# Kernel optimization log

Hardware: AMD Instinct MI355X
Metric: run time of the kernel (lower is better)

The kernel has to match this reference:

```python
import jax, jax.numpy as jnp
import numpy as np

N = 100000   # nodes
E = 1250000  # directed edges
F = 32       # node_features
H = 64       # hidden_channels
C = 10       # num_classes
NEG_SLOPE = 0.2  # GATConv default LeakyReLU slope


def _glorot(key, shape):
    fan_in = shape[0]
    return jax.random.normal(key, shape, jnp.float32) / np.sqrt(fan_in)


def setup_inputs() -> dict:
    k = jax.random.split(jax.random.key(0), 16)
    x = jax.random.normal(k[0], (N, F), jnp.float32)
    edge_index = jax.random.randint(k[1], (2, E), 0, N, dtype=jnp.int32)
    return {
        "x": x,
        "edge_index": edge_index,
        # GCNConv 1
        "W1": _glorot(k[2], (F, H)), "b1": jnp.zeros((H,), jnp.float32),
        # GATConv (heads=1)
        "W2": _glorot(k[3], (H, H)),
        "a_src": _glorot(k[4], (H,)), "a_dst": _glorot(k[5], (H,)),
        "b2": jnp.zeros((H,), jnp.float32),
        # GCNConv 3
        "W3": _glorot(k[6], (H, H)), "b3": jnp.zeros((H,), jnp.float32),
        # optimization head
        "Wopt": _glorot(k[7], (H, C)), "bopt": jnp.zeros((C,), jnp.float32),
        # bottleneck detector MLP
        "Wb1": _glorot(k[8], (H, 32)), "bb1": jnp.zeros((32,), jnp.float32),
        "Wb2": _glorot(k[9], (32, 1)), "bb2": jnp.zeros((1,), jnp.float32),
    }


def _gcn_conv(x, W, b, src, dst, n):
    # PyG GCNConv: self-loops already appended to src/dst by caller.
    h = x @ W  # [n, out]
    deg = jnp.zeros((n,), x.dtype).at[dst].add(1.0)
    dinv = jax.lax.rsqrt(jnp.maximum(deg, 1e-12))
    norm = dinv[src] * dinv[dst]  # [e]
    msg = h[src] * norm[:, None]  # gather + scale
    out = jnp.zeros_like(h).at[dst].add(msg)  # scatter-add
    return out + b


def _gat_conv(x, W, a_src, a_dst, b, src, dst, n):
    # PyG GATConv, heads=1: self-loops already appended.
    h = x @ W  # [n, out]
    alpha_s = h @ a_src  # [n]
    alpha_d = h @ a_dst  # [n]
    e = jax.nn.leaky_relu(alpha_s[src] + alpha_d[dst], NEG_SLOPE)  # [e]
    # softmax over incoming edges of each dst node
    emax = jax.ops.segment_max(e, dst, num_segments=n)
    p = jnp.exp(e - emax[dst])
    denom = jax.ops.segment_sum(p, dst, num_segments=n)
    alpha = p / denom[dst]
    out = jnp.zeros_like(h).at[dst].add(h[src] * alpha[:, None])
    return out + b


def reference(x, edge_index, W1, b1, W2, a_src, a_dst, b2, W3, b3,
              Wopt, bopt, Wb1, bb1, Wb2, bb2):
    n = x.shape[0]
    loops = jnp.arange(n, dtype=edge_index.dtype)
    src = jnp.concatenate([edge_index[0], loops])
    dst = jnp.concatenate([edge_index[1], loops])

    h = jax.nn.relu(_gcn_conv(x, W1, b1, src, dst, n))
    h = jax.nn.relu(_gat_conv(h, W2, a_src, a_dst, b2, src, dst, n))
    h = jax.nn.relu(_gcn_conv(h, W3, b3, src, dst, n))

    optimizations = h @ Wopt + bopt                     # [n, C]
    bottlenecks = jax.nn.sigmoid(jax.nn.relu(h @ Wb1 + bb1) @ Wb2 + bb2)  # [n, 1]
    graph_embedding = h.mean(axis=0)                    # [H]
    return optimizations, bottlenecks, graph_embedding
```

## Files before the change

kernel.cpp:

```cpp
#include <hip/hip_runtime.h>
#include <hip/hip_bf16.h>


#define CAP 64
#define NBUK 8

typedef unsigned uvec4 __attribute__((ext_vector_type(4)));

__device__ __forceinline__ int uwave(){
  return __builtin_amdgcn_readfirstlane(threadIdx.x >> 6);
}
__device__ __forceinline__ unsigned short f2bf(float f){
  unsigned u = __float_as_uint(f);
  return (unsigned short)((u + 0x7fffu + ((u >> 16) & 1u)) >> 16);
}
__device__ __forceinline__ float bfl(unsigned u){ return __uint_as_float(u << 16); }
__device__ __forceinline__ float bfh(unsigned u){ return __uint_as_float(u & 0xffff0000u); }

__global__ void k_setup(const float* __restrict__ Wopt, const float* __restrict__ bopt,
                        const float* __restrict__ Wb1, const float* __restrict__ bb1,
                        float* __restrict__ Wcat, float* __restrict__ bcat,
                        int* __restrict__ cnt, int* __restrict__ bcnt,
                        unsigned short* __restrict__ tb,
                        unsigned short* __restrict__ xh, float* __restrict__ emb_acc,
                        int n){
  int i = blockIdx.x*blockDim.x + threadIdx.x;
  if (i < n) cnt[i] = 0;
  if (blockIdx.x == 0){
    int tid = threadIdx.x;
    for (int j = tid; j < 4096; j += 256){
      int f = j >> 6, c = j & 63;
      float w = 0.f;
      if (c < 10)       w = Wopt[f*10 + c];
      else if (c >= 32) w = Wb1[f*32 + (c-32)];
      Wcat[j] = w;
    }
    if (tid < 64){
      float b = 0.f;
      if (tid < 10)       b = bopt[tid];
      else if (tid >= 32) b = bb1[tid-32];
      bcat[tid] = b;
      tb[(size_t)n*64 + tid] = 0;
      emb_acc[tid] = 0.f;
    }
    if (tid >= 64 && tid < 96) xh[(size_t)n*32 + (tid-64)] = 0;
    if (tid >= 96 && tid < 96 + NBUK) bcnt[tid-96] = 0;
  }
}

__global__ __launch_bounds__(256) void k_part(const int* __restrict__ src,
                        const int* __restrict__ dst,
                        uint2* __restrict__ pairs, int* __restrict__ bcnt,
                        int e, int pbcap, float binv){
  __shared__ int lcnt[NBUK];
  __shared__ int lbase[NBUK];
  int tid = threadIdx.x;
  if (tid < NBUK) lcnt[tid] = 0;
  __syncthreads();
  int i0 = blockIdx.x*1024 + tid*4;
  int d[4], s[4], bk[4], lp[4];
  int nv = e - i0;
  if (nv > 4) nv = 4;
  if (nv == 4){
    int4 dd = *(const int4*)(dst + i0);
    int4 ss = *(const int4*)(src + i0);
    d[0]=dd.x; d[1]=dd.y; d[2]=dd.z; d[3]=dd.w;
    s[0]=ss.x; s[1]=ss.y; s[2]=ss.z; s[3]=ss.w;
  } else {
    #pragma unroll
    for (int j = 0; j < 4; j++){ d[j] = 0; s[j] = 0; }
    for (int j = 0; j < nv; j++){ d[j] = dst[i0+j]; s[j] = src[i0+j]; }
  }
  #pragma unroll
  for (int j = 0; j < 4; j++){
    if (j < nv){
      bk[j] = min(NBUK-1, (int)((float)d[j] * binv));
      lp[j] = atomicAdd(&lcnt[bk[j]], 1);
    }
  }
  __syncthreads();
  if (tid < NBUK) lbase[tid] = atomicAdd(&bcnt[tid], lcnt[tid]);
  __syncthreads();
  #pragma unroll
  for (int j = 0; j < 4; j++){
    if (j < nv){
      int p = lbase[bk[j]] + lp[j];
      if (p < pbcap)
        pairs[(size_t)bk[j]*pbcap + p] = make_uint2((unsigned)d[j], (unsigned)s[j]);
    }
  }
}

__global__ __launch_bounds__(256) void k_fill(const uint2* __restrict__ pairs,
                        const int* __restrict__ bcnt, int* __restrict__ cnt,
                        int* __restrict__ adj, int pbcap){
  int b = blockIdx.x & (NBUK-1);
  int m = bcnt[b];
  if (m > pbcap) m = pbcap;
  const uvec4* pb = (const uvec4*)(pairs + (size_t)b*pbcap);
  int half = (m + 1) >> 1;
  int tpb = (gridDim.x >> 3) * 256;
  for (int j = (blockIdx.x >> 3)*256 + threadIdx.x; j < half; j += tpb){
    uvec4 p = __builtin_nontemporal_load(pb + j);
    int pos0 = atomicAdd(&cnt[p.x], 1);
    bool ok1 = (2*j + 1) < m;
    int pos1 = ok1 ? atomicAdd(&cnt[p.z], 1) : 0;
    if (pos0 < CAP) adj[(size_t)p.x*CAP + pos0] = (int)p.y;
    if (ok1 && pos1 < CAP) adj[(size_t)p.z*CAP + pos1] = (int)p.w;
  }
}

__global__ void k_castscale(const float* __restrict__ x, const int* __restrict__ cnt,
                            unsigned short* __restrict__ xh, int total4){
  int i = blockIdx.x*blockDim.x + threadIdx.x;
  if (i >= total4) return;
  int row = i >> 3;
  float dv = rsqrtf((float)(cnt[row] + 1));
  float4 v = ((const float4*)x)[i];
  uint2 o;
  o.x = (unsigned)f2bf(v.x*dv) | ((unsigned)f2bf(v.y*dv) << 16);
  o.y = (unsigned)f2bf(v.z*dv) | ((unsigned)f2bf(v.w*dv) << 16);
  ((uint2*)xh)[i] = o;
}

__global__ __launch_bounds__(256) void k_agg32g(const unsigned short* __restrict__ xh,
                          const int* __restrict__ adj, const int* __restrict__ cnt,
                          const float* __restrict__ W1, const float* __restrict__ b1,
                          unsigned short* __restrict__ h, int n){
  int lane = threadIdx.x & 63;
  float wreg[32];
  #pragma unroll
  for (int k = 0; k < 32; k++) wreg[k] = W1[k*64 + lane];
  float br = b1[lane];
  int v0 = blockIdx.x*8 + uwave()*2;
  if (v0 >= n) return;
  int v1 = v0 + 1;
  bool has1 = v1 < n;
  if (!has1) v1 = v0;
  int cn0 = cnt[v0], cn1 = cnt[v1];
  int c0 = min(cn0, CAP), c1 = min(cn1, CAP);
  int ureg0 = n, ureg1 = n;
  if (lane < c0) ureg0 = (adj + (size_t)v0*CAP)[lane];
  if (lane < c1) ureg1 = (adj + (size_t)v1*CAP)[lane];
  int g = lane >> 3, q = lane & 7;
  float4 a0 = {0.f,0.f,0.f,0.f}, a1 = {0.f,0.f,0.f,0.f};
  int itm = (max(c0, c1) + 7) >> 3;
  #pragma unroll 2
  for (int jj = 0; jj < itm; jj++){
    int u0 = __shfl(ureg0, jj*8 + g);
    int u1 = __shfl(ureg1, jj*8 + g);
    uint2 r0 = ((const uint2*)(xh + (size_t)u0*32))[q];
    uint2 r1 = ((const uint2*)(xh + (size_t)u1*32))[q];
    a0.x += bfl(r0.x); a0.y += bfh(r0.x); a0.z += bfl(r0.y); a0.w += bfh(r0.y);
    a1.x += bfl(r1.x); a1.y += bfh(r1.x); a1.z += bfl(r1.y); a1.w += bfh(r1.y);
  }
  #pragma unroll
  for (int off = 8; off <= 32; off <<= 1){
    a0.x += __shfl_xor(a0.x, off); a0.y += __shfl_xor(a0.y, off);
    a0.z += __shfl_xor(a0.z, off); a0.w += __shfl_xor(a0.w, off);
    a1.x += __shfl_xor(a1.x, off); a1.y += __shfl_xor(a1.y, off);
    a1.z += __shfl_xor(a1.z, off); a1.w += __shfl_xor(a1.w, off);
  }
  uint2 s0 = ((const uint2*)(xh + (size_t)v0*32))[q];
  uint2 s1 = ((const uint2*)(xh + (size_t)v1*32))[q];
  a0.x += bfl(s0.x); a0.y += bfh(s0.x); a0.z += bfl(s0.y); a0.w += bfh(s0.y);
  a1.x += bfl(s1.x); a1.y += bfh(s1.x); a1.z += bfl(s1.y); a1.w += bfh(s1.y);
  float dv0 = rsqrtf((float)(cn0 + 1)), dv1 = rsqrtf((float)(cn1 + 1));
  a0.x *= dv0; a0.y *= dv0; a0.z *= dv0; a0.w *= dv0;
  a1.x *= dv1; a1.y *= dv1; a1.z *= dv1; a1.w *= dv1;
  float h0 = br, h1v = br;
  #pragma unroll
  for (int q2 = 0; q2 < 8; q2++){
    float4 w0, w1;
    w0.x = __shfl(a0.x, q2); w0.y = __shfl(a0.y, q2);
    w0.z = __shfl(a0.z, q2); w0.w = __shfl(a0.w, q2);
    w1.x = __shfl(a1.x, q2); w1.y = __shfl(a1.y, q2);
    w1.z = __shfl(a1.z, q2); w1.w = __shfl(a1.w, q2);
    h0 = fmaf(w0.x, wreg[q2*4+0], h0); h1v = fmaf(w1.x, wreg[q2*4+0], h1v);
    h0 = fmaf(w0.y, wreg[q2*4+1], h0); h1v = fmaf(w1.y, wreg[q2*4+1], h1v);
    h0 = fmaf(w0.z, wreg[q2*4+2], h0); h1v = fmaf(w1.z, wreg[q2*4+2], h1v);
    h0 = fmaf(w0.w, wreg[q2*4+3], h0); h1v = fmaf(w1.w, wreg[q2*4+3], h1v);
  }
  h[(size_t)v0*64 + lane] = f2bf(fmaxf(h0, 0.f));
  if (has1) h[(size_t)v1*64 + lane] = f2bf(fmaxf(h1v, 0.f));
}

template<bool SCALE>
__global__ __launch_bounds__(256, 4) void k_gemm_b(const unsigned short* __restrict__ x,
                       const float* __restrict__ W, const int* __restrict__ cnt,
                       unsigned short* __restrict__ t, int n){
  int lane = threadIdx.x & 63;
  int gw = blockIdx.x*4 + uwave();
  int nw = gridDim.x*4;
  float wreg[64];
  #pragma unroll
  for (int k = 0; k < 64; k++) wreg[k] = W[k*64 + lane];
  for (int v = gw; v < n; v += nw){
    const uint4* xr = (const uint4*)(x + (size_t)v*64);
    float acc = 0.f;
    #pragma unroll
    for (int k8 = 0; k8 < 8; k8++){
      uint4 c = xr[k8];
      acc = fmaf(bfl(c.x), wreg[k8*8+0], acc);
      acc = fmaf(bfh(c.x), wreg[k8*8+1], acc);
      acc = fmaf(bfl(c.y), wreg[k8*8+2], acc);
      acc = fmaf(bfh(c.y), wreg[k8*8+3], acc);
      acc = fmaf(bfl(c.z), wreg[k8*8+4], acc);
      acc = fmaf(bfh(c.z), wreg[k8*8+5], acc);
      acc = fmaf(bfl(c.w), wreg[k8*8+6], acc);
      acc = fmaf(bfh(c.w), wreg[k8*8+7], acc);
    }
    if (SCALE) acc *= rsqrtf((float)(cnt[v] + 1));
    t[(size_t)v*64 + lane] = f2bf(acc);
  }
}

__global__ __launch_bounds__(256, 4) void k_gemm_alpha(const unsigned short* __restrict__ x,
                       const float* __restrict__ W,
                       const float* __restrict__ asrc, const float* __restrict__ adst,
                       unsigned short* __restrict__ t, float* __restrict__ als,
                       float* __restrict__ ald, int n){
  int lane = threadIdx.x & 63;
  int gw = blockIdx.x*4 + uwave();
  int nw = gridDim.x*4;
  float wreg[64];
  #pragma unroll
  for (int k = 0; k < 64; k++) wreg[k] = W[k*64 + lane];
  float asr = asrc[lane], adr = adst[lane];
  for (int v = gw; v < n; v += nw){
    const uint4* xr = (const uint4*)(x + (size_t)v*64);
    float acc = 0.f;
    #pragma unroll
    for (int k8 = 0; k8 < 8; k8++){
      uint4 c = xr[k8];
      acc = fmaf(bfl(c.x), wreg[k8*8+0], acc);
      acc = fmaf(bfh(c.x), wreg[k8*8+1], acc);
      acc = fmaf(bfl(c.y), wreg[k8*8+2], acc);
      acc = fmaf(bfh(c.y), wreg[k8*8+3], acc);
      acc = fmaf(bfl(c.z), wreg[k8*8+4], acc);
      acc = fmaf(bfh(c.z), wreg[k8*8+5], acc);
      acc = fmaf(bfl(c.w), wreg[k8*8+6], acc);
      acc = fmaf(bfh(c.w), wreg[k8*8+7], acc);
    }
    t[(size_t)v*64 + lane] = f2bf(acc);
    float s1 = acc * asr, s2 = acc * adr;
    #pragma unroll
    for (int off = 32; off; off >>= 1){
      s1 += __shfl_xor(s1, off);
      s2 += __shfl_xor(s2, off);
    }
    if (lane == 0){ als[v] = s1; ald[v] = s2; }
  }
}

__global__ __launch_bounds__(256) void k_gcn_agg(const unsigned short* __restrict__ t,
                          const int* __restrict__ adj, const int* __restrict__ cnt,
                          const float* __restrict__ b, unsigned short* __restrict__ h, int n){
  int lane = threadIdx.x & 63;
  int v0 = blockIdx.x*8 + uwave()*2;
  if (v0 >= n) return;
  int v1 = v0 + 1;
  bool has1 = v1 < n;
  if (!has1) v1 = v0;
  int cn0 = cnt[v0], cn1 = cnt[v1];
  int c0 = min(cn0, CAP), c1 = min(cn1, CAP);
  int ureg0 = n, ureg1 = n;
  if (lane < c0) ureg0 = (adj + (size_t)v0*CAP)[lane];
  if (lane < c1) ureg1 = (adj + (size_t)v1*CAP)[lane];
  int g = lane >> 3, q = lane & 7;
  float a0[8] = {0,0,0,0,0,0,0,0}, a1[8] = {0,0,0,0,0,0,0,0};
  int itm = (max(c0, c1) + 7) >> 3;
  #pragma unroll 2
  for (int jj = 0; jj < itm; jj++){
    int u0 = __shfl(ureg0, jj*8 + g);
    int u1 = __shfl(ureg1, jj*8 + g);
    uint4 r0 = ((const uint4*)(t + (size_t)u0*64))[q];
    uint4 r1 = ((const uint4*)(t + (size_t)u1*64))[q];
    a0[0] += bfl(r0.x); a0[1] += bfh(r0.x); a0[2] += bfl(r0.y); a0[3] += bfh(r0.y);
    a0[4] += bfl(r0.z); a0[5] += bfh(r0.z); a0[6] += bfl(r0.w); a0[7] += bfh(r0.w);
    a1[0] += bfl(r1.x); a1[1] += bfh(r1.x); a1[2] += bfl(r1.y); a1[3] += bfh(r1.y);
    a1[4] += bfl(r1.z); a1[5] += bfh(r1.z); a1[6] += bfl(r1.w); a1[7] += bfh(r1.w);
  }
  #pragma unroll
  for (int off = 8; off <= 32; off <<= 1){
    #pragma unroll
    for (int k = 0; k < 8; k++){
      a0[k] += __shfl_xor(a0[k], off);
      a1[k] += __shfl_xor(a1[k], off);
    }
  }
  uint4 s0 = ((const uint4*)(t + (size_t)v0*64))[q];
  uint4 s1 = ((const uint4*)(t + (size_t)v1*64))[q];
  a0[0] += bfl(s0.x); a0[1] += bfh(s0.x); a0[2] += bfl(s0.y); a0[3] += bfh(s0.y);
  a0[4] += bfl(s0.z); a0[5] += bfh(s0.z); a0[6] += bfl(s0.w); a0[7] += bfh(s0.w);
  a1[0] += bfl(s1.x); a1[1] += bfh(s1.x); a1[2] += bfl(s1.y); a1[3] += bfh(s1.y);
  a1[4] += bfl(s1.z); a1[5] += bfh(s1.z); a1[6] += bfl(s1.w); a1[7] += bfh(s1.w);
  float dv0 = rsqrtf((float)(cn0 + 1)), dv1 = rsqrtf((float)(cn1 + 1));
  float4 b0 = ((const float4*)b)[2*q], b1v = ((const float4*)b)[2*q+1];
  if (g == 0){
    float r0 = fmaxf(fmaf(a0[0], dv0, b0.x), 0.f),  r1 = fmaxf(fmaf(a0[1], dv0, b0.y), 0.f);
    float r2 = fmaxf(fmaf(a0[2], dv0, b0.z), 0.f),  r3 = fmaxf(fmaf(a0[3], dv0, b0.w), 0.f);
    float r4 = fmaxf(fmaf(a0[4], dv0, b1v.x), 0.f), r5 = fmaxf(fmaf(a0[5], dv0, b1v.y), 0.f);
    float r6 = fmaxf(fmaf(a0[6], dv0, b1v.z), 0.f), r7 = fmaxf(fmaf(a0[7], dv0, b1v.w), 0.f);
    uint4 o;
    o.x = (unsigned)f2bf(r0) | ((unsigned)f2bf(r1) << 16);
    o.y = (unsigned)f2bf(r2) | ((unsigned)f2bf(r3) << 16);
    o.z = (unsigned)f2bf(r4) | ((unsigned)f2bf(r5) << 16);
    o.w = (unsigned)f2bf(r6) | ((unsigned)f2bf(r7) << 16);
    ((uint4*)(h + (size_t)v0*64))[q] = o;
  } else if (g == 1 && has1){
    float r0 = fmaxf(fmaf(a1[0], dv1, b0.x), 0.f),  r1 = fmaxf(fmaf(a1[1], dv1, b0.y), 0.f);
    float r2 = fmaxf(fmaf(a1[2], dv1, b0.z), 0.f),  r3 = fmaxf(fmaf(a1[3], dv1, b0.w), 0.f);
    float r4 = fmaxf(fmaf(a1[4], dv1, b1v.x), 0.f), r5 = fmaxf(fmaf(a1[5], dv1, b1v.y), 0.f);
    float r6 = fmaxf(fmaf(a1[6], dv1, b1v.z), 0.f), r7 = fmaxf(fmaf(a1[7], dv1, b1v.w), 0.f);
    uint4 o;
    o.x = (unsigned)f2bf(r0) | ((unsigned)f2bf(r1) << 16);
    o.y = (unsigned)f2bf(r2) | ((unsigned)f2bf(r3) << 16);
    o.z = (unsigned)f2bf(r4) | ((unsigned)f2bf(r5) << 16);
    o.w = (unsigned)f2bf(r6) | ((unsigned)f2bf(r7) << 16);
    ((uint4*)(h + (size_t)v1*64))[q] = o;
  }
}

__global__ __launch_bounds__(256) void k_gat_agg(const unsigned short* __restrict__ t,
                          const int* __restrict__ adj, const int* __restrict__ cnt,
                          const float* __restrict__ als, const float* __restrict__ ald,
                          const float* __restrict__ b, unsigned short* __restrict__ h, int n){
  int lane = threadIdx.x & 63;
  int v0 = blockIdx.x*8 + uwave()*2;
  if (v0 >= n) return;
  int v1 = v0 + 1;
  bool has1 = v1 < n;
  if (!has1) v1 = v0;
  int c0 = min(cnt[v0], CAP), c1 = min(cnt[v1], CAP);
  int ureg0 = n, ureg1 = n;
  if (lane < c0) ureg0 = (adj + (size_t)v0*CAP)[lane];
  if (lane < c1) ureg1 = (adj + (size_t)v1*CAP)[lane];
  int us0 = (lane < c0) ? ureg0 : v0;
  int us1 = (lane < c1) ? ureg1 : v1;
  float adv0 = ald[v0], adv1 = ald[v1];
  float e0 = als[us0] + adv0;
  float e1 = als[us1] + adv1;
  e0 = e0 > 0.f ? e0 : 0.2f*e0;
  e1 = e1 > 0.f ? e1 : 0.2f*e1;
  float es0 = als[v0] + adv0; es0 = es0 > 0.f ? es0 : 0.2f*es0;
  float es1 = als[v1] + adv1; es1 = es1 > 0.f ? es1 : 0.2f*es1;
  float em0 = (lane < c0) ? e0 : -1e30f;
  float em1 = (lane < c1) ? e1 : -1e30f;
  #pragma unroll
  for (int off = 32; off; off >>= 1){
    em0 = fmaxf(em0, __shfl_xor(em0, off));
    em1 = fmaxf(em1, __shfl_xor(em1, off));
  }
  em0 = fmaxf(em0, es0); em1 = fmaxf(em1, es1);
  float p0 = (lane < c0) ? __expf(e0 - em0) : 0.f;
  float p1 = (lane < c1) ? __expf(e1 - em1) : 0.f;
  float sm0 = p0, sm1 = p1;
  #pragma unroll
  for (int off = 32; off; off >>= 1){
    sm0 += __shfl_xor(sm0, off);
    sm1 += __shfl_xor(sm1, off);
  }
  float ps0 = __expf(es0 - em0), ps1 = __expf(es1 - em1);
  float inv0 = 1.f / (sm0 + ps0), inv1 = 1.f / (sm1 + ps1);
  int g = lane >> 3, q = lane & 7;
  float a0[8] = {0,0,0,0,0,0,0,0}, a1[8] = {0,0,0,0,0,0,0,0};
  int itm = (max(c0, c1) + 7) >> 3;
  #pragma unroll 2
  for (int jj = 0; jj < itm; jj++){
    int   u0 = __shfl(ureg0, jj*8 + g);
    int   u1 = __shfl(ureg1, jj*8 + g);
    float w0 = __shfl(p0,    jj*8 + g);
    float w1 = __shfl(p1,    jj*8 + g);
    uint4 r0 = ((const uint4*)(t + (size_t)u0*64))[q];
    uint4 r1 = ((const uint4*)(t + (size_t)u1*64))[q];
    a0[0] = fmaf(w0, bfl(r0.x), a0[0]); a0[1] = fmaf(w0, bfh(r0.x), a0[1]);
    a0[2] = fmaf(w0, bfl(r0.y), a0[2]); a0[3] = fmaf(w0, bfh(r0.y), a0[3]);
    a0[4] = fmaf(w0, bfl(r0.z), a0[4]); a0[5] = fmaf(w0, bfh(r0.z), a0[5]);
    a0[6] = fmaf(w0, bfl(r0.w), a0[6]); a0[7] = fmaf(w0, bfh(r0.w), a0[7]);
    a1[0] = fmaf(w1, bfl(r1.x), a1[0]); a1[1] = fmaf(w1, bfh(r1.x), a1[1]);
    a1[2] = fmaf(w1, bfl(r1.y), a1[2]); a1[3] = fmaf(w1, bfh(r1.y), a1[3]);
    a1[4] = fmaf(w1, bfl(r1.z), a1[4]); a1[5] = fmaf(w1, bfh(r1.z), a1[5]);
    a1[6] = fmaf(w1, bfl(r1.w), a1[6]); a1[7] = fmaf(w1, bfh(r1.w), a1[7]);
  }
  #pragma unroll
  for (int off = 8; off <= 32; off <<= 1){
    #pragma unroll
    for (int k = 0; k < 8; k++){
      a0[k] += __shfl_xor(a0[k], off);
      a1[k] += __shfl_xor(a1[k], off);
    }
  }
  uint4 s0 = ((const uint4*)(t + (size_t)v0*64))[q];
  uint4 s1 = ((const uint4*)(t + (size_t)v1*64))[q];
  a0[0] = fmaf(ps0, bfl(s0.x), a0[0]); a0[1] = fmaf(ps0, bfh(s0.x), a0[1]);
  a0[2] = fmaf(ps0, bfl(s0.y), a0[2]); a0[3] = fmaf(ps0, bfh(s0.y), a0[3]);
  a0[4] = fmaf(ps0, bfl(s0.z), a0[4]); a0[5] = fmaf(ps0, bfh(s0.z), a0[5]);
  a0[6] = fmaf(ps0, bfl(s0.w), a0[6]); a0[7] = fmaf(ps0, bfh(s0.w), a0[7]);
  a1[0] = fmaf(ps1, bfl(s1.x), a1[0]); a1[1] = fmaf(ps1, bfh(s1.x), a1[1]);
  a1[2] = fmaf(ps1, bfl(s1.y), a1[2]); a1[3] = fmaf(ps1, bfh(s1.y), a1[3]);
  a1[4] = fmaf(ps1, bfl(s1.z), a1[4]); a1[5] = fmaf(ps1, bfh(s1.z), a1[5]);
  a1[6] = fmaf(ps1, bfl(s1.w), a1[6]); a1[7] = fmaf(ps1, bfh(s1.w), a1[7]);
  float4 b0 = ((const float4*)b)[2*q], b1v = ((const float4*)b)[2*q+1];
  if (g == 0){
    float r0 = fmaxf(fmaf(a0[0], inv0, b0.x), 0.f),  r1 = fmaxf(fmaf(a0[1], inv0, b0.y), 0.f);
    float r2 = fmaxf(fmaf(a0[2], inv0, b0.z), 0.f),  r3 = fmaxf(fmaf(a0[3], inv0, b0.w), 0.f);
    float r4 = fmaxf(fmaf(a0[4], inv0, b1v.x), 0.f), r5 = fmaxf(fmaf(a0[5], inv0, b1v.y), 0.f);
    float r6 = fmaxf(fmaf(a0[6], inv0, b1v.z), 0.f), r7 = fmaxf(fmaf(a0[7], inv0, b1v.w), 0.f);
    uint4 o;
    o.x = (unsigned)f2bf(r0) | ((unsigned)f2bf(r1) << 16);
    o.y = (unsigned)f2bf(r2) | ((unsigned)f2bf(r3) << 16);
    o.z = (unsigned)f2bf(r4) | ((unsigned)f2bf(r5) << 16);
    o.w = (unsigned)f2bf(r6) | ((unsigned)f2bf(r7) << 16);
    ((uint4*)(h + (size_t)v0*64))[q] = o;
  } else if (g == 1 && has1){
    float r0 = fmaxf(fmaf(a1[0], inv1, b0.x), 0.f),  r1 = fmaxf(fmaf(a1[1], inv1, b0.y), 0.f);
    float r2 = fmaxf(fmaf(a1[2], inv1, b0.z), 0.f),  r3 = fmaxf(fmaf(a1[3], inv1, b0.w), 0.f);
    float r4 = fmaxf(fmaf(a1[4], inv1, b1v.x), 0.f), r5 = fmaxf(fmaf(a1[5], inv1, b1v.y), 0.f);
    float r6 = fmaxf(fmaf(a1[6], inv1, b1v.z), 0.f), r7 = fmaxf(fmaf(a1[7], inv1, b1v.w), 0.f);
    uint4 o;
    o.x = (unsigned)f2bf(r0) | ((unsigned)f2bf(r1) << 16);
    o.y = (unsigned)f2bf(r2) | ((unsigned)f2bf(r3) << 16);
    o.z = (unsigned)f2bf(r4) | ((unsigned)f2bf(r5) << 16);
    o.w = (unsigned)f2bf(r6) | ((unsigned)f2bf(r7) << 16);
    ((uint4*)(h + (size_t)v1*64))[q] = o;
  }
}

__global__ __launch_bounds__(256, 4) void k_heads(const unsigned short* __restrict__ h,
                        const float* __restrict__ Wcat, const float* __restrict__ bcat,
                        const float* __restrict__ Wb2, const float* __restrict__ bb2,
                        float* __restrict__ out_opt, float* __restrict__ out_bot, int n){
  int lane = threadIdx.x & 63;
  int gw = blockIdx.x*4 + uwave();
  int nw = gridDim.x*4;
  float wreg[64];
  #pragma unroll
  for (int k = 0; k < 64; k++) wreg[k] = Wcat[k*64 + lane];
  float bcr  = bcat[lane];
  float wb2r = (lane >= 32) ? Wb2[lane-32] : 0.f;
  float bb2r = bb2[0];
  for (int v = gw; v < n; v += nw){
    const uint4* xr = (const uint4*)(h + (size_t)v*64);
    float acc = bcr;
    #pragma unroll
    for (int k8 = 0; k8 < 8; k8++){
      uint4 c = xr[k8];
      acc = fmaf(bfl(c.x), wreg[k8*8+0], acc);
      acc = fmaf(bfh(c.x), wreg[k8*8+1], acc);
      acc = fmaf(bfl(c.y), wreg[k8*8+2], acc);
      acc = fmaf(bfh(c.y), wreg[k8*8+3], acc);
      acc = fmaf(bfl(c.z), wreg[k8*8+4], acc);
      acc = fmaf(bfh(c.z), wreg[k8*8+5], acc);
      acc = fmaf(bfl(c.w), wreg[k8*8+6], acc);
      acc = fmaf(bfh(c.w), wreg[k8*8+7], acc);
    }
    if (lane < 10) out_opt[(size_t)v*10 + lane] = acc;
    float contrib = fmaxf(acc, 0.f) * wb2r;
    #pragma unroll
    for (int off = 32; off; off >>= 1) contrib += __shfl_xor(contrib, off);
    if (lane == 0) out_bot[v] = 1.f / (1.f + __expf(-(contrib + bb2r)));
  }
}

__global__ __launch_bounds__(256) void k_mean(const unsigned short* __restrict__ h,
                       float* __restrict__ emb_acc, int n){
  __shared__ float red[256];
  int tid = threadIdx.x;
  int w = tid >> 6, lane = tid & 63;
  float s = 0.f;
  for (int r = blockIdx.x*4 + w; r < n; r += 1024)
    s += __uint_as_float(((unsigned)h[(size_t)r*64 + lane]) << 16);
  red[tid] = s;
  __syncthreads();
  if (tid < 64)
    atomicAdd(&emb_acc[tid], red[tid] + red[64+tid] + red[128+tid] + red[192+tid]);
}

__global__ void k_embed(const float* __restrict__ emb_acc, float* __restrict__ out_emb,
                        float invn){
  if (threadIdx.x < 64) out_emb[threadIdx.x] = emb_acc[threadIdx.x] * invn;
}

extern "C" void kernel_launch(void* const* d_in, const int* in_sizes, int n_in,
                              void* d_out, int out_size, void* d_ws, size_t ws_size,
                              hipStream_t stream) {
  const float* x    = (const float*)d_in[0];
  const int*   ei   = (const int*)d_in[1];
  const float* W1   = (const float*)d_in[2];
  const float* b1   = (const float*)d_in[3];
  const float* W2   = (const float*)d_in[4];
  const float* a_s  = (const float*)d_in[5];
  const float* a_d  = (const float*)d_in[6];
  const float* b2   = (const float*)d_in[7];
  const float* W3   = (const float*)d_in[8];
  const float* b3   = (const float*)d_in[9];
  const float* Wopt = (const float*)d_in[10];
  const float* bopt = (const float*)d_in[11];
  const float* Wb1  = (const float*)d_in[12];
  const float* bb1  = (const float*)d_in[13];
  const float* Wb2  = (const float*)d_in[14];
  const float* bb2  = (const float*)d_in[15];

  int n = in_sizes[0] / 32;
  int e = in_sizes[1] / 2;
  const int* src = ei;
  const int* dst = ei + e;

  char* ws = (char*)d_ws;
  size_t off = 0;
  auto alloc = [&](size_t bytes) -> void* {
    void* p = ws + off;
    off += (bytes + 255) & ~(size_t)255;
    return p;
  };
  int*            cnt     = (int*)           alloc((size_t)n * 4);
  int*            adj     = (int*)           alloc((size_t)n * CAP * 4);
  float*          als     = (float*)         alloc((size_t)n * 4);
  float*          ald     = (float*)         alloc((size_t)n * 4);
  unsigned short* xh      = (unsigned short*)alloc((size_t)(n+1) * 32 * 2);
  unsigned short* tb      = (unsigned short*)alloc((size_t)(n+1) * 64 * 2);
  unsigned short* hbuf    = (unsigned short*)alloc((size_t)n * 64 * 2);
  float*          emb_acc = (float*)         alloc((size_t)64 * 4);
  float*          Wcat    = (float*)         alloc((size_t)4096 * 4);
  float*          bcat    = (float*)         alloc((size_t)64 * 4);
  int*            bcnt    = (int*)           alloc((size_t)NBUK * 4);

  int pbcap = e / NBUK + 8192;
  uint2* pairs = (uint2*)hbuf;

  float* out_opt = (float*)d_out;
  float* out_bot = out_opt + (size_t)n * 10;
  float* out_emb = out_bot + n;

  int nb8    = (n + 7) / 8;
  int nbN    = (n + 255) / 256;
  int nbP    = (e + 1023) / 1024;
  int total4 = n*32/4;
  int nbC    = (total4 + 255) / 256;

  k_setup<<<nbN, 256, 0, stream>>>(Wopt, bopt, Wb1, bb1, Wcat, bcat,
                                   cnt, bcnt, tb, xh, emb_acc, n);
  k_part<<<nbP, 256, 0, stream>>>(src, dst, pairs, bcnt, e, pbcap, 8.0f/(float)n);
  k_fill<<<2048, 256, 0, stream>>>(pairs, bcnt, cnt, adj, pbcap);
  k_castscale<<<nbC, 256, 0, stream>>>(x, cnt, xh, total4);

  k_agg32g<<<nb8, 256, 0, stream>>>(xh, adj, cnt, W1, b1, hbuf, n);

  k_gemm_alpha<<<1024, 256, 0, stream>>>(hbuf, W2, a_s, a_d, tb, als, ald, n);
  k_gat_agg<<<nb8, 256, 0, stream>>>(tb, adj, cnt, als, ald, b2, hbuf, n);

  k_gemm_b<true><<<1024, 256, 0, stream>>>(hbuf, W3, cnt, tb, n);
  k_gcn_agg<<<nb8, 256, 0, stream>>>(tb, adj, cnt, b3, hbuf, n);

  k_heads<<<1024, 256, 0, stream>>>(hbuf, Wcat, bcat, Wb2, bb2,
                                    out_opt, out_bot, n);
  k_mean<<<256, 256, 0, stream>>>(hbuf, emb_acc, n);
  k_embed<<<1, 64, 0, stream>>>(emb_acc, out_emb, 1.0f / (float)n);
}
```

Measured before the change: 413.2 us.

## Partition edges into 128-node buckets and build adjacency in shared memory

The edge partition step now buckets edges by dst>>7 into about 782 fine buckets instead of 8 coarse ones. Each fill block then builds its 128 nodes' counts and adjacency lists with LDS atomics and writes them to global memory with coalesced vector stores. This replaces global atomics on cnt and scattered adjacency writes, and removes the separate cnt zeroing. The costs are 32KB of LDS per fill block (lower occupancy), more global bucket-counter atomics in the partition step, and a tighter per-bucket pair capacity that could overflow on skewed graphs.

```diff
diff --git a/kernel.cpp b/kernel.cpp
--- a/kernel.cpp
+++ b/kernel.cpp
@@ -3,9 +3,8 @@
 
 
 #define CAP 64
-#define NBUK 8
-
-typedef unsigned uvec4 __attribute__((ext_vector_type(4)));
+#define NP2 128
+#define NB2MAX 800
 
 __device__ __forceinline__ int uwave(){
   return __builtin_amdgcn_readfirstlane(threadIdx.x >> 6);
@@ -20,12 +19,11 @@
 __global__ void k_setup(const float* __restrict__ Wopt, const float* __restrict__ bopt,
                         const float* __restrict__ Wb1, const float* __restrict__ bb1,
                         float* __restrict__ Wcat, float* __restrict__ bcat,
-                        int* __restrict__ cnt, int* __restrict__ bcnt,
-                        unsigned short* __restrict__ tb,
+                        int* __restrict__ bcnt, unsigned short* __restrict__ tb,
                         unsigned short* __restrict__ xh, float* __restrict__ emb_acc,
-                        int n){
+                        int n, int nb2){
   int i = blockIdx.x*blockDim.x + threadIdx.x;
-  if (i < n) cnt[i] = 0;
+  if (i < nb2) bcnt[i] = 0;
   if (blockIdx.x == 0){
     int tid = threadIdx.x;
     for (int j = tid; j < 4096; j += 256){
@@ -44,45 +42,50 @@
       emb_acc[tid] = 0.f;
     }
     if (tid >= 64 && tid < 96) xh[(size_t)n*32 + (tid-64)] = 0;
-    if (tid >= 96 && tid < 96 + NBUK) bcnt[tid-96] = 0;
   }
 }
 
 __global__ __launch_bounds__(256) void k_part(const int* __restrict__ src,
                         const int* __restrict__ dst,
                         uint2* __restrict__ pairs, int* __restrict__ bcnt,
-                        int e, int pbcap, float binv){
-  __shared__ int lcnt[NBUK];
-  __shared__ int lbase[NBUK];
+                        int e, int nb2, int pbcap){
+  __shared__ int lcnt[NB2MAX];
+  __shared__ int lbase[NB2MAX];
   int tid = threadIdx.x;
-  if (tid < NBUK) lcnt[tid] = 0;
+  for (int j = tid; j < nb2; j += 256) lcnt[j] = 0;
   __syncthreads();
-  int i0 = blockIdx.x*1024 + tid*4;
-  int d[4], s[4], bk[4], lp[4];
+  int i0 = blockIdx.x*2048 + tid*8;
+  int d[8], s[8], bk[8], lp[8];
   int nv = e - i0;
-  if (nv > 4) nv = 4;
-  if (nv == 4){
-    int4 dd = *(const int4*)(dst + i0);
-    int4 ss = *(const int4*)(src + i0);
-    d[0]=dd.x; d[1]=dd.y; d[2]=dd.z; d[3]=dd.w;
-    s[0]=ss.x; s[1]=ss.y; s[2]=ss.z; s[3]=ss.w;
+  if (nv > 8) nv = 8;
+  if (nv < 0) nv = 0;
+  if (nv == 8){
+    int4 d0 = *(const int4*)(dst + i0), d1 = *(const int4*)(dst + i0 + 4);
+    int4 s0 = *(const int4*)(src + i0), s1 = *(const int4*)(src + i0 + 4);
+    d[0]=d0.x; d[1]=d0.y; d[2]=d0.z; d[3]=d0.w;
+    d[4]=d1.x; d[5]=d1.y; d[6]=d1.z; d[7]=d1.w;
+    s[0]=s0.x; s[1]=s0.y; s[2]=s0.z; s[3]=s0.w;
+    s[4]=s1.x; s[5]=s1.y; s[6]=s1.z; s[7]=s1.w;
   } else {
     #pragma unroll
-    for (int j = 0; j < 4; j++){ d[j] = 0; s[j] = 0; }
+    for (int j = 0; j < 8; j++){ d[j] = 0; s[j] = 0; }
     for (int j = 0; j < nv; j++){ d[j] = dst[i0+j]; s[j] = src[i0+j]; }
   }
   #pragma unroll
-  for (int j = 0; j < 4; j++){
+  for (int j = 0; j < 8; j++){
     if (j < nv){
-      bk[j] = min(NBUK-1, (int)((float)d[j] * binv));
+      bk[j] = d[j] >> 7;
       lp[j] = atomicAdd(&lcnt[bk[j]], 1);
     }
   }
   __syncthreads();
-  if (tid < NBUK) lbase[tid] = atomicAdd(&bcnt[tid], lcnt[tid]);
+  for (int j = tid; j < nb2; j += 256){
+    int c = lcnt[j];
+    if (c) lbase[j] = atomicAdd(&bcnt[j], c);
+  }
   __syncthreads();
   #pragma unroll
-  for (int j = 0; j < 4; j++){
+  for (int j = 0; j < 8; j++){
     if (j < nv){
       int p = lbase[bk[j]] + lp[j];
       if (p < pbcap)
@@ -93,21 +96,30 @@
 
 __global__ __launch_bounds__(256) void k_fill(const uint2* __restrict__ pairs,
                         const int* __restrict__ bcnt, int* __restrict__ cnt,
-                        int* __restrict__ adj, int pbcap){
-  int b = blockIdx.x & (NBUK-1);
+                        int* __restrict__ adj, int pbcap, int n){
+  __shared__ int lc[NP2];
+  __shared__ int ladj[NP2*CAP];
+  int b = blockIdx.x;
+  int lo = b << 7;
+  int nn = min(NP2, n - lo);
+  int tid = threadIdx.x;
+  for (int j = tid; j < NP2; j += 256) lc[j] = 0;
+  __syncthreads();
   int m = bcnt[b];
   if (m > pbcap) m = pbcap;
-  const uvec4* pb = (const uvec4*)(pairs + (size_t)b*pbcap);
-  int half = (m + 1) >> 1;
-  int tpb = (gridDim.x >> 3) * 256;
-  for (int j = (blockIdx.x >> 3)*256 + threadIdx.x; j < half; j += tpb){
-    uvec4 p = __builtin_nontemporal_load(pb + j);
-    int pos0 = atomicAdd(&cnt[p.x], 1);
-    bool ok1 = (2*j + 1) < m;
-    int pos1 = ok1 ? atomicAdd(&cnt[p.z], 1) : 0;
-    if (pos0 < CAP) adj[(size_t)p.x*CAP + pos0] = (int)p.y;
-    if (ok1 && pos1 < CAP) adj[(size_t)p.z*CAP + pos1] = (int)p.w;
-  }
+  const uint2* pb = pairs + (size_t)b*pbcap;
+  for (int j = tid; j < m; j += 256){
+    uint2 p = pb[j];
+    int r = (int)p.x - lo;
+    int pos = atomicAdd(&lc[r], 1);
+    if (pos < CAP) ladj[(r << 6) + pos] = (int)p.y;
+  }
+  __syncthreads();
+  if (tid < nn) cnt[lo + tid] = lc[tid];
+  int tot = nn << 4;
+  uint4* ga = (uint4*)(adj + (size_t)lo*CAP);
+  const uint4* la = (const uint4*)ladj;
+  for (int j = tid; j < tot; j += 256) ga[j] = la[j];
 }
 
 __global__ void k_castscale(const float* __restrict__ x, const int* __restrict__ cnt,
@@ -514,6 +526,7 @@
     off += (bytes + 255) & ~(size_t)255;
     return p;
   };
+  int nb2 = (n + NP2 - 1) >> 7;
   int*            cnt     = (int*)           alloc((size_t)n * 4);
   int*            adj     = (int*)           alloc((size_t)n * CAP * 4);
   float*          als     = (float*)         alloc((size_t)n * 4);
@@ -524,9 +537,11 @@
   float*          emb_acc = (float*)         alloc((size_t)64 * 4);
   float*          Wcat    = (float*)         alloc((size_t)4096 * 4);
   float*          bcat    = (float*)         alloc((size_t)64 * 4);
-  int*            bcnt    = (int*)           alloc((size_t)NBUK * 4);
-
-  int pbcap = e / NBUK + 8192;
+  int*            bcnt    = (int*)           alloc((size_t)nb2 * 4);
+
+  int pbcap = e / nb2 + 384;
+  long pcap_max = ((long)n * 128) / ((long)nb2 * 8);
+  if (pbcap > (int)pcap_max) pbcap = (int)pcap_max;
   uint2* pairs = (uint2*)hbuf;
 
   float* out_opt = (float*)d_out;
@@ -535,14 +550,14 @@
 
   int nb8    = (n + 7) / 8;
   int nbN    = (n + 255) / 256;
-  int nbP    = (e + 1023) / 1024;
+  int nbP    = (e + 2047) / 2048;
   int total4 = n*32/4;
   int nbC    = (total4 + 255) / 256;
 
   k_setup<<<nbN, 256, 0, stream>>>(Wopt, bopt, Wb1, bb1, Wcat, bcat,
-                                   cnt, bcnt, tb, xh, emb_acc, n);
-  k_part<<<nbP, 256, 0, stream>>>(src, dst, pairs, bcnt, e, pbcap, 8.0f/(float)n);
-  k_fill<<<2048, 256, 0, stream>>>(pairs, bcnt, cnt, adj, pbcap);
+                                   bcnt, tb, xh, emb_acc, n, nb2);
+  k_part<<<nbP, 256, 0, stream>>>(src, dst, pairs, bcnt, e, nb2, pbcap);
+  k_fill<<<nb2, 256, 0, stream>>>(pairs, bcnt, cnt, adj, pbcap, n);
   k_castscale<<<nbC, 256, 0, stream>>>(x, cnt, xh, total4);
 
   k_agg32g<<<nb8, 256, 0, stream>>>(xh, adj, cnt, W1, b1, hbuf, n);
```

Result: faster. 377.3 us (-8.7%).
